# Optimization experiments

Measured on AMD Instinct MI355X. Metric: run time of the kernel, lower is better.

The kernel has to match this reference:

```python
import jax, jax.numpy as jnp
import numpy as np

# Config (matches init_kwargs / input_specs)
H = 128      # hidden_dim
D = 3        # depth (atom message-passing steps)
L = 2        # layers (molecule readout steps)
N = 100000   # total nodes in batch
E = 400000   # total directed edges
G = 5000     # number of graphs (molecules)
FN = 64      # num_atom_type
FE = 16      # num_bond_type


def setup_inputs() -> dict:
    key = jax.random.key(0)
    ks = jax.random.split(key, 32)
    rn = lambda k, shape, s=0.1: jax.random.normal(k, shape, jnp.float32) * s
    inp = {
        'node': rn(ks[0], (N, FN), 1.0),
        'edge': rn(ks[1], (E, FE), 1.0),
        'src': jax.random.randint(ks[2], (E,), 0, N),
        'dst': jax.random.randint(ks[3], (E,), 0, N),
        'graph_ids': jnp.sort(jax.random.randint(ks[4], (N,), 0, G)),
        # input embeddings
        'Wn0': rn(ks[5], (FN, H)), 'bn0': rn(ks[6], (H,)),
        'We0': rn(ks[7], (FE, H)), 'be0': rn(ks[8], (H,)),
        # Atom_AFPLayer params, stacked over depth D
        'aWn': rn(ks[9], (D, H, H)),      'abn': rn(ks[10], (D, H)),
        'aWe': rn(ks[11], (D, 2 * H, H)), 'abe': rn(ks[12], (D, H)),
        'aWal': rn(ks[13], (D, 2 * H, 1)),'abal': rn(ks[14], (D, 1)),
        'aWat': rn(ks[15], (D, H, H)),    'abat': rn(ks[16], (D, H)),
        'aWih': rn(ks[17], (D, H, 3 * H)),'abih': rn(ks[18], (D, 3 * H)),
        'aWhh': rn(ks[19], (D, H, 3 * H)),'abhh': rn(ks[20], (D, 3 * H)),
        # Mol_AFPLayer params, stacked over L
        'mWal': rn(ks[21], (L, 2 * H, 1)),'mbal': rn(ks[22], (L, 1)),
        'mWat': rn(ks[23], (L, H, H)),    'mbat': rn(ks[24], (L, H)),
        'mWih': rn(ks[25], (L, H, 3 * H)),'mbih': rn(ks[26], (L, 3 * H)),
        'mWhh': rn(ks[27], (L, H, 3 * H)),'mbhh': rn(ks[28], (L, 3 * H)),
        # final predictor
        'Wp': rn(ks[29], (H, 1)), 'bp': rn(ks[30], (1,)),
    }
    return inp


def _gru(x, h, Wih, bih, Whh, bhh):
    # torch.nn.GRUCell gate order: r, z, n
    gi = x @ Wih + bih
    gh = h @ Whh + bhh
    ir, iz, inn = jnp.split(gi, 3, axis=-1)
    hr, hz, hn = jnp.split(gh, 3, axis=-1)
    r = jax.nn.sigmoid(ir + hr)
    z = jax.nn.sigmoid(iz + hz)
    n = jnp.tanh(inn + r * hn)
    return (1.0 - z) * n + z * h


def _seg_softmax(score, seg, num):
    # numerically stable softmax within each segment; score: [E,1]
    m = jax.ops.segment_max(score, seg, num_segments=num)
    e = jnp.exp(score - m[seg])
    s = jax.ops.segment_sum(e, seg, num_segments=num)
    return e / s[seg]


def _forward(node, edge, src, dst, graph_ids,
             Wn0, bn0, We0, be0,
             aWn, abn, aWe, abe, aWal, abal, aWat, abat,
             aWih, abih, aWhh, abhh,
             mWal, mbal, mWat, mbat, mWih, mbih, mWhh, mbhh,
             Wp, bp):
    lrelu = jax.nn.leaky_relu  # slope 0.01, same as torch default
    n = lrelu(node @ Wn0 + bn0)   # [N,H] embedded nodes
    e = lrelu(edge @ We0 + be0)   # [E,H] embedded edges (constant across steps)
    Nn = n.shape[0]
    # Atom-level attentive message passing (depth D), per-layer weights
    for d in range(D):
        h = lrelu(n @ aWn[d] + abn[d])                                        # node_embedded_feats
        msg = lrelu(jnp.concatenate([h[src], e], -1) @ aWe[d] + abe[d])       # [E,H] neighbor_message
        score = lrelu(jnp.concatenate([msg, h[dst]], -1) @ aWal[d] + abal[d]) # [E,1]
        att = _seg_softmax(score, dst, Nn)                                    # edge_softmax over dst
        ctx = jax.ops.segment_sum(att * (msg @ aWat[d] + abat[d]), dst, num_segments=Nn)
        ctx = jax.nn.elu(ctx)
        n = jax.nn.relu(_gru(ctx, h, aWih[d], abih[d], aWhh[d], abhh[d]))
    # Molecule-level attentive readout (L steps)
    sn = jax.ops.segment_sum(n, graph_ids, num_segments=G)  # dgl.sum_nodes init
    for l in range(L):
        s = lrelu(sn)
        sc = lrelu(jnp.concatenate([n, s[graph_ids]], -1) @ mWal[l] + mbal[l])  # [N,1]
        aw = _seg_softmax(sc, graph_ids, G)                                     # softmax_nodes
        hid = n @ mWat[l] + mbat[l]
        sctx = jax.nn.elu(jax.ops.segment_sum(aw * hid, graph_ids, num_segments=G))
        sn = jax.nn.relu(_gru(sctx, s, mWih[l], mbih[l], mWhh[l], mbhh[l]))
    return sn @ Wp + bp  # [G,1]


def reference(node, edge, src, dst, graph_ids,
              Wn0, bn0, We0, be0,
              aWn, abn, aWe, abe, aWal, abal, aWat, abat,
              aWih, abih, aWhh, abhh,
              mWal, mbal, mWat, mbat, mWih, mbih, mWhh, mbhh,
              Wp, bp):
    return _forward(node, edge, src, dst, graph_ids,
                    Wn0, bn0, We0, be0,
                    aWn, abn, aWe, abe, aWal, abal, aWat, abat,
                    aWih, abih, aWhh, abhh,
                    mWal, mbal, mWat, mbat, mWih, mbih, mWhh, mbhh,
                    Wp, bp)
```

## Files before the change

kernel.cpp:

```cpp
#include <hip/hip_runtime.h>
#include <hip/hip_bf16.h>
#include <math.h>


#define HD 128
#define H3 384

typedef __attribute__((ext_vector_type(8))) short short8;
typedef __attribute__((ext_vector_type(4))) float f32x4;

__device__ __forceinline__ float lrelu_f(float x) { return x > 0.f ? x : 0.01f * x; }
__device__ __forceinline__ float sigmoid_f(float x) { return 1.f / (1.f + expf(-x)); }

__device__ __forceinline__ void atomicMaxF(float* addr, float val) {
    int iv = __float_as_int(val);
    if (iv >= 0) atomicMax((int*)addr, iv);
    else atomicMin((unsigned int*)addr, (unsigned int)iv);
}

__device__ __forceinline__ unsigned short bf16_rne(float v, float* back) {
    unsigned u = __float_as_uint(v);
    unsigned r = (u + 0x7FFFu + ((u >> 16) & 1u)) >> 16;
    *back = __uint_as_float(r << 16);
    return (unsigned short)r;
}

__device__ __forceinline__ unsigned pack_hl(float v) {
    float back, d;
    unsigned short h = bf16_rne(v, &back);
    unsigned short l = bf16_rne(v - back, &d);
    return ((unsigned)h << 16) | (unsigned)l;
}
__device__ __forceinline__ float unpack_f32(unsigned w) {
    return __uint_as_float(w & 0xffff0000u) + __uint_as_float(w << 16);
}

__device__ __forceinline__ void split8(const float* p, short8& h8, short8& l8) {
    float4 u0 = *reinterpret_cast<const float4*>(p);
    float4 u1 = *reinterpret_cast<const float4*>(p + 4);
    float vv[8] = {u0.x, u0.y, u0.z, u0.w, u1.x, u1.y, u1.z, u1.w};
#pragma unroll
    for (int j = 0; j < 8; ++j) {
        float back, d;
        h8[j] = (short)bf16_rne(vv[j], &back);
        l8[j] = (short)bf16_rne(vv[j] - back, &d);
    }
}

__device__ __forceinline__ void unpack8(const unsigned* p, short8& h8, short8& l8) {
    uint4 w0 = *reinterpret_cast<const uint4*>(p);
    uint4 w1 = *reinterpret_cast<const uint4*>(p + 4);
    unsigned ww[8] = {w0.x, w0.y, w0.z, w0.w, w1.x, w1.y, w1.z, w1.w};
#pragma unroll
    for (int j = 0; j < 8; ++j) {
        h8[j] = (short)(ww[j] >> 16);
        l8[j] = (short)(ww[j] & 0xffffu);
    }
}

__global__ void pack_b_kernel(const float* __restrict__ B, int K, int ldb, int col0,
                              int Ncols, short* __restrict__ hi, short* __restrict__ lo,
                              size_t matB, size_t matO) {
    int KG = 4 * ((K + 31) / 32);
    int mat = blockIdx.y;
    B += (size_t)mat * matB;
    hi += (size_t)mat * matO;
    lo += (size_t)mat * matO;
    int idx = blockIdx.x * blockDim.x + threadIdx.x;
    int total = (Ncols >> 4) * KG * 16;
    if (idx >= total) return;
    int col = idx & 15;
    int kg = (idx >> 4) % KG;
    int nblk = idx / (16 * KG);
    size_t o = (size_t)idx * 8;
#pragma unroll
    for (int e = 0; e < 8; ++e) {
        int k = kg * 8 + e;
        float v = (k < K) ? B[(size_t)k * ldb + col0 + nblk * 16 + col] : 0.f;
        float hf, d;
        unsigned short h = bf16_rne(v, &hf);
        unsigned short l = bf16_rne(v - hf, &d);
        hi[o + e] = (short)h;
        lo[o + e] = (short)l;
    }
}

#define GRU_SL (8 * 16 * 16 * 8)
__global__ void pack_gru_kernel(const float* __restrict__ Wih, const float* __restrict__ Whh,
                                int D, short* __restrict__ hi, short* __restrict__ lo) {
    const int per = 6 * (GRU_SL / 8);
    int idx = blockIdx.x * blockDim.x + threadIdx.x;
    if (idx >= D * per) return;
    int d = idx / per;
    int r = idx % per;
    int s = r / (GRU_SL / 8);
    int g8 = r % (GRU_SL / 8);
    int col = g8 & 15;
    int kg = (g8 >> 4) & 15;
    int nblk = g8 >> 8;
    const float* B = (s < 3 ? Wih : Whh) + (size_t)d * HD * H3;
    int col0 = (s % 3) * HD;
    size_t o = (size_t)idx * 8;
#pragma unroll
    for (int e = 0; e < 8; ++e) {
        int k = kg * 8 + e;
        float v = B[(size_t)k * H3 + col0 + nblk * 16 + col];
        float hf, d2;
        unsigned short h = bf16_rne(v, &hf);
        unsigned short l = bf16_rne(v - hf, &d2);
        hi[o + e] = (short)h;
        lo[o + e] = (short)l;
    }
}

__global__ __launch_bounds__(256) void mfma_gemm(
    const float* __restrict__ A, int K,
    const short* __restrict__ Bhi, const short* __restrict__ Blo, int KG,
    const float* __restrict__ bias, float* __restrict__ C, int M, int N, int act,
    const float* __restrict__ rdw, float* __restrict__ rdout,
    const float* __restrict__ rowmask, int outpk, int apk)
{
    const int t = threadIdx.x, lane = t & 63, w = t >> 6;
    const int wm = w & 1, wn = w >> 1, q = lane >> 4, r16 = lane & 15;
    const int m0 = blockIdx.x * 64, n0 = blockIdx.y * 64;
    const int KT = K >> 5;

    f32x4 acc[2][2];
#pragma unroll
    for (int a = 0; a < 2; ++a)
#pragma unroll
        for (int b = 0; b < 2; ++b) { acc[a][b][0]=0.f; acc[a][b][1]=0.f; acc[a][b][2]=0.f; acc[a][b][3]=0.f; }

    int arow[2];
#pragma unroll
    for (int mt = 0; mt < 2; ++mt) {
        int m = m0 + (wm << 5) + (mt << 4) + r16;
        arow[mt] = (m >= M) ? M - 1 : m;
    }

    for (int kt = 0; kt < KT; ++kt) {
        short8 ah[2], al[2];
#pragma unroll
        for (int mt = 0; mt < 2; ++mt) {
            size_t aoff = (size_t)arow[mt] * K + (kt << 5) + (q << 3);
            if (apk) unpack8((const unsigned*)A + aoff, ah[mt], al[mt]);
            else split8(A + aoff, ah[mt], al[mt]);
        }
        const int kg = (kt << 2) + q;
#pragma unroll
        for (int nt = 0; nt < 2; ++nt) {
            int nblk = (n0 >> 4) + (wn << 1) + nt;
            size_t boff = (((size_t)nblk * KG + kg) * 16 + r16) * 8;
            short8 bh = *reinterpret_cast<const short8*>(Bhi + boff);
            short8 bl = *reinterpret_cast<const short8*>(Blo + boff);
#pragma unroll
            for (int mt = 0; mt < 2; ++mt) {
                acc[mt][nt] = __builtin_amdgcn_mfma_f32_16x16x32_bf16(ah[mt], bh, acc[mt][nt], 0, 0, 0);
                acc[mt][nt] = __builtin_amdgcn_mfma_f32_16x16x32_bf16(ah[mt], bl, acc[mt][nt], 0, 0, 0);
                acc[mt][nt] = __builtin_amdgcn_mfma_f32_16x16x32_bf16(al[mt], bh, acc[mt][nt], 0, 0, 0);
            }
        }
    }

#pragma unroll
    for (int mt = 0; mt < 2; ++mt) {
        float pv[4] = {0.f, 0.f, 0.f, 0.f};
#pragma unroll
        for (int nt = 0; nt < 2; ++nt) {
            int col = n0 + (wn << 5) + (nt << 4) + r16;
            float bi = bias ? bias[col] : 0.f;
            float wc = rdw ? rdw[col] : 0.f;
#pragma unroll
            for (int i = 0; i < 4; ++i) {
                int m = m0 + (wm << 5) + (mt << 4) + (q << 2) + i;
                float v = acc[mt][nt][i] + bi;
                if (act == 1) v = v > 0.f ? v : 0.01f * v;
                else if (act == 2) v = fmaxf(v, 0.f);
                else if (act == 3) v = v > 0.f ? v : expf(v) - 1.f;
                if (rowmask && m < M && rowmask[m] == 0.f) v = 0.f;
                pv[i] += wc * v;
                if (m < M) {
                    if (outpk) ((unsigned*)C)[(size_t)m * N + col] = pack_hl(v);
                    else C[(size_t)m * N + col] = v;
                }
            }
        }
        if (rdw) {
#pragma unroll
            for (int i = 0; i < 4; ++i) {
                float p = pv[i];
                p += __shfl_xor(p, 1); p += __shfl_xor(p, 2);
                p += __shfl_xor(p, 4); p += __shfl_xor(p, 8);
                int m = m0 + (wm << 5) + (mt << 4) + (q << 2) + i;
                if (r16 == 0 && m < M) atomicAdd(&rdout[m], p);
            }
        }
    }
}

__global__ __launch_bounds__(256) void msg_pass_kernel(
    const unsigned* __restrict__ hpk, const int* __restrict__ srcp,
    const int* __restrict__ dstp, const int* __restrict__ eidp,
    const float* __restrict__ edge,
    const short* __restrict__ W0hi, const short* __restrict__ W0lo,
    const float* __restrict__ be0,
    const short* __restrict__ Wehi, const short* __restrict__ Welo,
    const float* __restrict__ be,
    const float* __restrict__ wal,
    float* __restrict__ sc, float* __restrict__ S,
    void* __restrict__ msgpk, int fullprec,
    int E, int mode)
{
    __shared__ unsigned int elds[64 * 128];
    const int t = threadIdx.x, lane = t & 63, w = t >> 6;
    const int wm = w & 1, wn = w >> 1, q = lane >> 4, r16 = lane & 15;
    const int e0 = blockIdx.x * 64;

    {
        f32x4 ea[2][4];
#pragma unroll
        for (int a = 0; a < 2; ++a)
#pragma unroll
            for (int b = 0; b < 4; ++b) { ea[a][b][0]=0.f; ea[a][b][1]=0.f; ea[a][b][2]=0.f; ea[a][b][3]=0.f; }
        short8 eah[2], eal[2];
#pragma unroll
        for (int mt = 0; mt < 2; ++mt) {
            int er = e0 + (wm << 5) + (mt << 4) + r16;
            if (er >= E) er = E - 1;
            int eid = eidp[er];
            if (q < 2) split8(edge + (size_t)eid * 16 + (q << 3), eah[mt], eal[mt]);
            else {
#pragma unroll
                for (int j = 0; j < 8; ++j) { eah[mt][j] = 0; eal[mt][j] = 0; }
            }
        }
#pragma unroll
        for (int nt = 0; nt < 4; ++nt) {
            int nblk = (wn << 2) + nt;
            size_t boff = (((size_t)nblk * 4 + q) * 16 + r16) * 8;
            short8 bh = *reinterpret_cast<const short8*>(W0hi + boff);
            short8 bl = *reinterpret_cast<const short8*>(W0lo + boff);
#pragma unroll
            for (int mt = 0; mt < 2; ++mt) {
                ea[mt][nt] = __builtin_amdgcn_mfma_f32_16x16x32_bf16(eah[mt], bh, ea[mt][nt], 0, 0, 0);
                ea[mt][nt] = __builtin_amdgcn_mfma_f32_16x16x32_bf16(eah[mt], bl, ea[mt][nt], 0, 0, 0);
                ea[mt][nt] = __builtin_amdgcn_mfma_f32_16x16x32_bf16(eal[mt], bh, ea[mt][nt], 0, 0, 0);
            }
        }
#pragma unroll
        for (int mt = 0; mt < 2; ++mt)
#pragma unroll
            for (int nt = 0; nt < 4; ++nt) {
                int col = (wn << 6) + (nt << 4) + r16;
#pragma unroll
                for (int i = 0; i < 4; ++i) {
                    int row = (wm << 5) + (mt << 4) + (q << 2) + i;
                    float v = lrelu_f(ea[mt][nt][i] + be0[col]);
                    elds[row * 128 + (col ^ ((row & 7) << 2))] = pack_hl(v);
                }
            }
    }
    __syncthreads();

    f32x4 acc[2][4];
#pragma unroll
    for (int a = 0; a < 2; ++a)
#pragma unroll
        for (int b = 0; b < 4; ++b) { acc[a][b][0]=0.f; acc[a][b][1]=0.f; acc[a][b][2]=0.f; acc[a][b][3]=0.f; }
    int grow[2], arw[2];
#pragma unroll
    for (int mt = 0; mt < 2; ++mt) {
        int m = e0 + (wm << 5) + (mt << 4) + r16;
        if (m >= E) m = E - 1;
        grow[mt] = srcp[m];
        arw[mt] = (wm << 5) + (mt << 4) + r16;
    }
#pragma unroll
    for (int kt = 0; kt < 8; ++kt) {
        short8 ah[2], al[2];
#pragma unroll
        for (int mt = 0; mt < 2; ++mt) {
            if (kt < 4) {
                unpack8(hpk + (size_t)grow[mt] * HD + (kt << 5) + (q << 3), ah[mt], al[mt]);
            } else {
                int row = arw[mt];
                int sh = (row & 7) << 2;
                int c = ((kt - 4) << 5) + (q << 3);
                uint4 w0 = *reinterpret_cast<const uint4*>(&elds[row * 128 + (c ^ sh)]);
                uint4 w1 = *reinterpret_cast<const uint4*>(&elds[row * 128 + ((c + 4) ^ sh)]);
                unsigned ww[8] = {w0.x, w0.y, w0.z, w0.w, w1.x, w1.y, w1.z, w1.w};
#pragma unroll
                for (int j = 0; j < 8; ++j) {
                    ah[mt][j] = (short)(ww[j] >> 16);
                    al[mt][j] = (short)(ww[j] & 0xffffu);
                }
            }
        }
        const int kg = (kt << 2) + q;
#pragma unroll
        for (int nt = 0; nt < 4; ++nt) {
            int nblk = (wn << 2) + nt;
            size_t boff = (((size_t)nblk * 32 + kg) * 16 + r16) * 8;
            short8 bh = *reinterpret_cast<const short8*>(Wehi + boff);
            short8 bl = *reinterpret_cast<const short8*>(Welo + boff);
#pragma unroll
            for (int mt = 0; mt < 2; ++mt) {
                acc[mt][nt] = __builtin_amdgcn_mfma_f32_16x16x32_bf16(ah[mt], bh, acc[mt][nt], 0, 0, 0);
                acc[mt][nt] = __builtin_amdgcn_mfma_f32_16x16x32_bf16(ah[mt], bl, acc[mt][nt], 0, 0, 0);
                acc[mt][nt] = __builtin_amdgcn_mfma_f32_16x16x32_bf16(al[mt], bh, acc[mt][nt], 0, 0, 0);
            }
        }
    }

    if (mode == 2) {
#pragma unroll
        for (int mt = 0; mt < 2; ++mt)
#pragma unroll
            for (int i = 0; i < 4; ++i) {
                int m = e0 + (wm << 5) + (mt << 4) + (q << 2) + i;
                if (m >= E) continue;
                float a = sc[m];
                int dn = dstp[m];
#pragma unroll
                for (int nt = 0; nt < 4; ++nt) {
                    int col = (wn << 6) + (nt << 4) + r16;
                    float v = lrelu_f(acc[mt][nt][i] + be[col]);
                    atomicAdd(&S[(size_t)dn * HD + col], a * v);
                }
            }
        return;
    }

#pragma unroll
    for (int mt = 0; mt < 2; ++mt) {
        float pv[4] = {0.f, 0.f, 0.f, 0.f};
#pragma unroll
        for (int i = 0; i < 4; ++i) {
            int m = e0 + (wm << 5) + (mt << 4) + (q << 2) + i;
#pragma unroll
            for (int nt = 0; nt < 4; ++nt) {
                int col = (wn << 6) + (nt << 4) + r16;
                float v = lrelu_f(acc[mt][nt][i] + be[col]);
                pv[i] += wal[col] * v;
                if (mode == 0 && m < E) {
                    size_t ro = (size_t)m * HD + col;
                    if (fullprec) ((unsigned*)msgpk)[ro] = pack_hl(v);
                    else { float b_; ((unsigned short*)msgpk)[ro] = bf16_rne(v, &b_); }
                }
            }
        }
#pragma unroll
        for (int i = 0; i < 4; ++i) {
            float p = pv[i];
            p += __shfl_xor(p, 1); p += __shfl_xor(p, 2);
            p += __shfl_xor(p, 4); p += __shfl_xor(p, 8);
            int m = e0 + (wm << 5) + (mt << 4) + (q << 2) + i;
            if (r16 == 0 && m < E) atomicAdd(&sc[m], p);
        }
    }
}

__global__ __launch_bounds__(256) void ctx_gather_kernel(
    const void* __restrict__ msgpk, const float* __restrict__ sc,
    const int* __restrict__ rowptr, unsigned* __restrict__ Spk, int Nn, int fullprec)
{
    int wid = (blockIdx.x * blockDim.x + threadIdx.x) >> 6;
    int lane = threadIdx.x & 63;
    if (wid >= Nn) return;
    int p0 = rowptr[wid], p1 = rowptr[wid + 1];
    float a0 = 0.f, a1 = 0.f;
    if (fullprec) {
        const unsigned* mp = (const unsigned*)msgpk;
        for (int p = p0; p < p1; ++p) {
            float a = sc[p];
            uint2 w = *reinterpret_cast<const uint2*>(mp + (size_t)p * HD + lane * 2);
            a0 += a * unpack_f32(w.x);
            a1 += a * unpack_f32(w.y);
        }
    } else {
        const unsigned short* mp = (const unsigned short*)msgpk;
        for (int p = p0; p < p1; ++p) {
            float a = sc[p];
            unsigned w = *reinterpret_cast<const unsigned*>(mp + (size_t)p * HD + lane * 2);
            a0 += a * __uint_as_float(w << 16);
            a1 += a * __uint_as_float(w & 0xffff0000u);
        }
    }
    Spk[(size_t)wid * HD + lane * 2] = pack_hl(a0);
    Spk[(size_t)wid * HD + lane * 2 + 1] = pack_hl(a1);
}

__global__ void hist_kernel(const int* __restrict__ dst, int* __restrict__ cnt, int E) {
    int i = blockIdx.x * blockDim.x + threadIdx.x;
    if (i < E) atomicAdd(&cnt[dst[i]], 1);
}
__global__ void scan1_kernel(const int* __restrict__ cnt, int* __restrict__ pre,
                             int* __restrict__ btot, int total) {
    __shared__ int ts[256];
    int base = blockIdx.x * 1024;
    int c[4], tsum = 0;
#pragma unroll
    for (int j = 0; j < 4; ++j) {
        int idx = base + threadIdx.x * 4 + j;
        c[j] = (idx < total) ? cnt[idx] : 0;
        tsum += c[j];
    }
    ts[threadIdx.x] = tsum;
    __syncthreads();
    for (int off = 1; off < 256; off <<= 1) {
        int v = (threadIdx.x >= off) ? ts[threadIdx.x - off] : 0;
        __syncthreads();
        ts[threadIdx.x] += v;
        __syncthreads();
    }
    int run = ts[threadIdx.x] - tsum;
#pragma unroll
    for (int j = 0; j < 4; ++j) {
        int idx = base + threadIdx.x * 4 + j;
        if (idx < total) pre[idx] = run;
        run += c[j];
    }
    if (threadIdx.x == 255) btot[blockIdx.x] = ts[255];
}
__global__ void scan2_kernel(int* __restrict__ btot, int nb) {
    __shared__ int ts[256];
    int v = (threadIdx.x < nb) ? btot[threadIdx.x] : 0;
    ts[threadIdx.x] = v;
    __syncthreads();
    for (int off = 1; off < 256; off <<= 1) {
        int u = (threadIdx.x >= off) ? ts[threadIdx.x - off] : 0;
        __syncthreads();
        ts[threadIdx.x] += u;
        __syncthreads();
    }
    if (threadIdx.x < nb) btot[threadIdx.x] = ts[threadIdx.x] - v;
}
__global__ void scan3_kernel(int* __restrict__ pre, const int* __restrict__ btot, int total) {
    int i = blockIdx.x * blockDim.x + threadIdx.x;
    if (i < total) pre[i] += btot[i >> 10];
}
__global__ void fill_kernel(const int* __restrict__ src, const int* __restrict__ dst,
                            const int* __restrict__ rowptr, int* __restrict__ fillc,
                            int* __restrict__ srcp, int* __restrict__ dstp,
                            int* __restrict__ eidp, int E) {
    int i = blockIdx.x * blockDim.x + threadIdx.x;
    if (i >= E) return;
    int d = dst[i];
    int pos = rowptr[d] + atomicAdd(&fillc[d], 1);
    srcp[pos] = src[i];
    dstp[pos] = d;
    eidp[pos] = i;
}

__global__ __launch_bounds__(256) void gru_fused_kernel(
    const unsigned* __restrict__ ctxpk, const unsigned* __restrict__ hpk,
    const short* __restrict__ ghi, const short* __restrict__ glo,
    const float* __restrict__ bih, const float* __restrict__ bhh,
    unsigned* __restrict__ out, int M)
{
    const int t = threadIdx.x, lane = t & 63, w = t >> 6;
    const int wm = w & 1, wn = w >> 1, q = lane >> 4, r16 = lane & 15;
    const int m0 = blockIdx.x * 64, j0 = blockIdx.y * 64;

    f32x4 acc[6][2][2];
#pragma unroll
    for (int g = 0; g < 6; ++g)
#pragma unroll
        for (int a = 0; a < 2; ++a)
#pragma unroll
            for (int b = 0; b < 2; ++b) { acc[g][a][b][0]=0.f; acc[g][a][b][1]=0.f; acc[g][a][b][2]=0.f; acc[g][a][b][3]=0.f; }

    int arow[2];
#pragma unroll
    for (int mt = 0; mt < 2; ++mt) {
        int m = m0 + (wm << 5) + (mt << 4) + r16;
        arow[mt] = (m >= M) ? M - 1 : m;
    }

#pragma unroll
    for (int kt = 0; kt < 4; ++kt) {
        short8 ah[2], al[2];
#pragma unroll
        for (int mt = 0; mt < 2; ++mt)
            unpack8(ctxpk + (size_t)arow[mt] * HD + (kt << 5) + (q << 3), ah[mt], al[mt]);
        const int kg = (kt << 2) + q;
#pragma unroll
        for (int g = 0; g < 3; ++g)
#pragma unroll
            for (int nt = 0; nt < 2; ++nt) {
                int nblk = (j0 >> 4) + (wn << 1) + nt;
                size_t boff = (size_t)g * GRU_SL + (((size_t)nblk * 16 + kg) * 16 + r16) * 8;
                short8 bh = *reinterpret_cast<const short8*>(ghi + boff);
                short8 bl = *reinterpret_cast<const short8*>(glo + boff);
#pragma unroll
                for (int mt = 0; mt < 2; ++mt) {
                    acc[g][mt][nt] = __builtin_amdgcn_mfma_f32_16x16x32_bf16(ah[mt], bh, acc[g][mt][nt], 0, 0, 0);
                    acc[g][mt][nt] = __builtin_amdgcn_mfma_f32_16x16x32_bf16(ah[mt], bl, acc[g][mt][nt], 0, 0, 0);
                    acc[g][mt][nt] = __builtin_amdgcn_mfma_f32_16x16x32_bf16(al[mt], bh, acc[g][mt][nt], 0, 0, 0);
                }
            }
    }
#pragma unroll
    for (int kt = 0; kt < 4; ++kt) {
        short8 ah[2], al[2];
#pragma unroll
        for (int mt = 0; mt < 2; ++mt)
            unpack8(hpk + (size_t)arow[mt] * HD + (kt << 5) + (q << 3), ah[mt], al[mt]);
        const int kg = (kt << 2) + q;
#pragma unroll
        for (int g = 3; g < 6; ++g)
#pragma unroll
            for (int nt = 0; nt < 2; ++nt) {
                int nblk = (j0 >> 4) + (wn << 1) + nt;
                size_t boff = (size_t)g * GRU_SL + (((size_t)nblk * 16 + kg) * 16 + r16) * 8;
                short8 bh = *reinterpret_cast<const short8*>(ghi + boff);
                short8 bl = *reinterpret_cast<const short8*>(glo + boff);
#pragma unroll
                for (int mt = 0; mt < 2; ++mt) {
                    acc[g][mt][nt] = __builtin_amdgcn_mfma_f32_16x16x32_bf16(ah[mt], bh, acc[g][mt][nt], 0, 0, 0);
                    acc[g][mt][nt] = __builtin_amdgcn_mfma_f32_16x16x32_bf16(ah[mt], bl, acc[g][mt][nt], 0, 0, 0);
                    acc[g][mt][nt] = __builtin_amdgcn_mfma_f32_16x16x32_bf16(al[mt], bh, acc[g][mt][nt], 0, 0, 0);
                }
            }
    }

#pragma unroll
    for (int mt = 0; mt < 2; ++mt)
#pragma unroll
        for (int nt = 0; nt < 2; ++nt) {
            int j = j0 + (wn << 5) + (nt << 4) + r16;
            float bir = bih[j], biz = bih[HD + j], bin = bih[2 * HD + j];
            float bhr = bhh[j], bhz = bhh[HD + j], bhn = bhh[2 * HD + j];
#pragma unroll
            for (int i = 0; i < 4; ++i) {
                int m = m0 + (wm << 5) + (mt << 4) + (q << 2) + i;
                if (m >= M) continue;
                float r = sigmoid_f(acc[0][mt][nt][i] + bir + acc[3][mt][nt][i] + bhr);
                float z = sigmoid_f(acc[1][mt][nt][i] + biz + acc[4][mt][nt][i] + bhz);
                float hn = acc[5][mt][nt][i] + bhn;
                float nn = tanhf(acc[2][mt][nt][i] + bin + r * hn);
                float hv = unpack_f32(hpk[(size_t)m * HD + j]);
                out[(size_t)m * HD + j] = pack_hl(fmaxf((1.f - z) * nn + z * hv, 0.f));
            }
        }
}

__global__ void init_maxsum_kernel(float* mx, float* sm, int n) {
    int i = blockIdx.x * blockDim.x + threadIdx.x;
    if (i < n) { mx[i] = -__builtin_inff(); sm[i] = 0.f; }
}

__global__ void score_combine_kernel(float* __restrict__ sc, const float* __restrict__ hd2,
                                     const int* __restrict__ seg, const float* __restrict__ bal,
                                     float* __restrict__ maxbuf, int count) {
    int i = blockIdx.x * blockDim.x + threadIdx.x;
    if (i >= count) return;
    int s = seg[i];
    float v = lrelu_f(sc[i] + hd2[s] + bal[0]);
    sc[i] = v;
    atomicMaxF(&maxbuf[s], v);
}

__global__ __launch_bounds__(256) void score_kernel(
    const unsigned* __restrict__ Apk, const float* __restrict__ B,
    const int* __restrict__ seg, const float* __restrict__ w,
    const float* __restrict__ bal, float* __restrict__ out,
    float* __restrict__ maxbuf, int count)
{
    int i = (blockIdx.x * blockDim.x + threadIdx.x) >> 6;
    int lane = threadIdx.x & 63;
    if (i >= count) return;
    int s = seg[i];
    float a0 = unpack_f32(Apk[(size_t)i * HD + lane]);
    float a1 = unpack_f32(Apk[(size_t)i * HD + lane + 64]);
    const float* br = B + (size_t)s * HD;
    float p = a0 * w[lane] + a1 * w[lane + 64]
            + br[lane] * w[128 + lane] + br[lane + 64] * w[192 + lane];
#pragma unroll
    for (int off = 32; off > 0; off >>= 1) p += __shfl_down(p, off);
    if (lane == 0) {
        float v = lrelu_f(p + bal[0]);
        out[i] = v;
        atomicMaxF(&maxbuf[s], v);
    }
}

__global__ void expsum_kernel(float* __restrict__ sc, const float* __restrict__ mx,
                              float* __restrict__ sm, const int* __restrict__ seg, int count) {
    int i = blockIdx.x * blockDim.x + threadIdx.x;
    if (i >= count) return;
    int s = seg[i];
    float p = expf(sc[i] - mx[s]);
    sc[i] = p;
    atomicAdd(&sm[s], p);
}

__global__ void attdiv_kernel(float* __restrict__ sc, const float* __restrict__ sm,
                              const int* __restrict__ seg, int count) {
    int i = blockIdx.x * blockDim.x + threadIdx.x;
    if (i >= count) return;
    sc[i] = sc[i] / sm[seg[i]];
}

__global__ void gru_gate_kernel(const float* __restrict__ gi, const float* __restrict__ gh,
                                const float* __restrict__ h, float* __restrict__ out, int M) {
    size_t idx = (size_t)blockIdx.x * blockDim.x + threadIdx.x;
    if (idx >= (size_t)M * HD) return;
    size_t row = idx >> 7; int col = (int)(idx & 127);
    const float* gir = gi + row * H3;
    const float* ghr = gh + row * H3;
    float r = sigmoid_f(gir[col] + ghr[col]);
    float z = sigmoid_f(gir[col + 128] + ghr[col + 128]);
    float nn = tanhf(gir[col + 256] + r * ghr[col + 256]);
    float o = (1.f - z) * nn + z * h[idx];
    out[idx] = fmaxf(o, 0.f);
}

__global__ void lrelu_copy_kernel(const float* __restrict__ in, float* __restrict__ out, size_t n) {
    size_t i = (size_t)blockIdx.x * blockDim.x + threadIdx.x;
    if (i >= n) return;
    out[i] = lrelu_f(in[i]);
}

__global__ void segsum_kernel(const unsigned* __restrict__ npk, const int* __restrict__ gid,
                              float* __restrict__ sn, int Nn) {
    size_t idx = (size_t)blockIdx.x * blockDim.x + threadIdx.x;
    if (idx >= (size_t)Nn * HD) return;
    size_t row = idx >> 7; int col = (int)(idx & 127);
    atomicAdd(&sn[(size_t)gid[row] * HD + col], unpack_f32(npk[idx]));
}

__global__ void seg_scale_sum_kernel(const unsigned* __restrict__ npk, const int* __restrict__ gid,
                                     const float* __restrict__ scale, float* __restrict__ out, int Nn) {
    size_t idx = (size_t)blockIdx.x * blockDim.x + threadIdx.x;
    if (idx >= (size_t)Nn * HD) return;
    size_t row = idx >> 7; int col = (int)(idx & 127);
    atomicAdd(&out[(size_t)gid[row] * HD + col], scale[row] * unpack_f32(npk[idx]));
}

__global__ void final_kernel(const float* __restrict__ sn, const float* __restrict__ Wp,
                             const float* __restrict__ bp, float* __restrict__ out, int G) {
    int g = (blockIdx.x * blockDim.x + threadIdx.x) >> 6;
    int lane = threadIdx.x & 63;
    if (g >= G) return;
    const float* r = sn + (size_t)g * HD;
    float p = r[lane] * Wp[lane] + r[lane + 64] * Wp[lane + 64];
#pragma unroll
    for (int off = 32; off > 0; off >>= 1) p += __shfl_down(p, off);
    if (lane == 0) out[g] = p + bp[0];
}

__global__ void canary_kernel(float* out, int n) {
    int i = blockIdx.x * blockDim.x + threadIdx.x;
    if (i < n) out[i] = 123.456f;
}

struct PkB { const short* hi; const short* lo; int KG; };

extern "C" void kernel_launch(void* const* d_in, const int* in_sizes, int n_in,
                              void* d_out, int out_size, void* d_ws, size_t ws_size,
                              hipStream_t stream) {
    const float* node = (const float*)d_in[0];
    const float* edge = (const float*)d_in[1];
    const int*   src  = (const int*)d_in[2];
    const int*   dst  = (const int*)d_in[3];
    const int*   gid  = (const int*)d_in[4];
    const float* Wn0  = (const float*)d_in[5];
    const float* bn0  = (const float*)d_in[6];
    const float* We0  = (const float*)d_in[7];
    const float* be0  = (const float*)d_in[8];
    const float* aWn  = (const float*)d_in[9];
    const float* abn  = (const float*)d_in[10];
    const float* aWe  = (const float*)d_in[11];
    const float* abe  = (const float*)d_in[12];
    const float* aWal = (const float*)d_in[13];
    const float* abal = (const float*)d_in[14];
    const float* aWat = (const float*)d_in[15];
    const float* abat = (const float*)d_in[16];
    const float* aWih = (const float*)d_in[17];
    const float* abih = (const float*)d_in[18];
    const float* aWhh = (const float*)d_in[19];
    const float* abhh = (const float*)d_in[20];
    const float* mWal = (const float*)d_in[21];
    const float* mbal = (const float*)d_in[22];
    const float* mWat = (const float*)d_in[23];
    const float* mbat = (const float*)d_in[24];
    const float* mWih = (const float*)d_in[25];
    const float* mbih = (const float*)d_in[26];
    const float* mWhh = (const float*)d_in[27];
    const float* mbhh = (const float*)d_in[28];
    const float* Wp   = (const float*)d_in[29];
    const float* bp   = (const float*)d_in[30];

    const int N = in_sizes[0] / 64;
    const int E = in_sizes[1] / 16;
    const int G = out_size;
    const int D = in_sizes[9] / (HD * HD);
    const int L = in_sizes[21] / (2 * HD);
    if (D > 8 || L > 4) return;

    char* wsb = (char*)d_ws;

    short* pkcur = (short*)wsb;
    size_t elN;
    auto packBn = [&](const float* B, int K, int ldb, int col0, int Ncols,
                      int nmat, size_t matB) -> PkB {
        int KG = 4 * ((K + 31) / 32);
        size_t elems = (size_t)(Ncols >> 4) * KG * 16 * 8;
        elN = elems;
        short* hi = pkcur; pkcur += elems * nmat;
        short* lo = pkcur; pkcur += elems * nmat;
        int total = (Ncols >> 4) * KG * 16;
        dim3 g((total + 255) / 256, nmat);
        pack_b_kernel<<<g, 256, 0, stream>>>(B, K, ldb, col0, Ncols, hi, lo, matB, elems);
        PkB p; p.hi = hi; p.lo = lo; p.KG = KG; return p;
    };
    PkB pWe0 = packBn(We0, 16, HD, 0, HD, 1, 0);
    PkB pWn0 = packBn(Wn0, 64, HD, 0, HD, 1, 0);
    PkB pAWn[8], pAWe[8], pAWat[8];
    {
        PkB b = packBn(aWn, HD, HD, 0, HD, D, (size_t)HD * HD);
        for (int d = 0; d < D; ++d) { pAWn[d] = b; pAWn[d].hi = b.hi + d * elN; pAWn[d].lo = b.lo + d * elN; }
        b = packBn(aWe, 2 * HD, HD, 0, HD, D, (size_t)2 * HD * HD);
        for (int d = 0; d < D; ++d) { pAWe[d] = b; pAWe[d].hi = b.hi + d * elN; pAWe[d].lo = b.lo + d * elN; }
        b = packBn(aWat, HD, HD, 0, HD, D, (size_t)HD * HD);
        for (int d = 0; d < D; ++d) { pAWat[d] = b; pAWat[d].hi = b.hi + d * elN; pAWat[d].lo = b.lo + d * elN; }
    }
    short* ghiAll = pkcur; pkcur += (size_t)D * 6 * GRU_SL;
    short* gloAll = pkcur; pkcur += (size_t)D * 6 * GRU_SL;
    {
        int total = D * 6 * (GRU_SL / 8);
        pack_gru_kernel<<<(total + 255) / 256, 256, 0, stream>>>(aWih, aWhh, D, ghiAll, gloAll);
    }
    const short *gHi[8], *gLo[8];
    for (int d = 0; d < D; ++d) {
        gHi[d] = ghiAll + (size_t)d * 6 * GRU_SL;
        gLo[d] = gloAll + (size_t)d * 6 * GRU_SL;
    }
    PkB pMWat[4], pMWih[4], pMWhh[4];
    {
        PkB b = packBn(mWat, HD, HD, 0, HD, L, (size_t)HD * HD);
        for (int l = 0; l < L; ++l) { pMWat[l] = b; pMWat[l].hi = b.hi + l * elN; pMWat[l].lo = b.lo + l * elN; }
        b = packBn(mWih, HD, H3, 0, H3, L, (size_t)HD * H3);
        for (int l = 0; l < L; ++l) { pMWih[l] = b; pMWih[l].hi = b.hi + l * elN; pMWih[l].lo = b.lo + l * elN; }
        b = packBn(mWhh, HD, H3, 0, H3, L, (size_t)HD * H3);
        for (int l = 0; l < L; ++l) { pMWhh[l] = b; pMWhh[l].hi = b.hi + l * elN; pMWhh[l].lo = b.lo + l * elN; }
    }

    size_t off = ((size_t)((char*)pkcur - wsb) + 255) & ~(size_t)255;
    auto alloc = [&](size_t bytes) -> void* {
        void* p = (void*)(wsb + off);
        off += (bytes + 255) & ~(size_t)255;
        return p;
    };
    unsigned* npk = (unsigned*)alloc((size_t)N * HD * 4);
    unsigned* hpk = (unsigned*)alloc((size_t)N * HD * 4);
    float* sc_e = (float*)alloc((size_t)E * 4);
    float* nmax = (float*)alloc((size_t)N * 4);
    float* nsum = (float*)alloc((size_t)N * 4);
    float* sc_n = (float*)alloc((size_t)N * 4);
    float* hd2  = (float*)alloc((size_t)N * 4);
    float* sn   = (float*)alloc((size_t)G * HD * 4);
    float* gmax = (float*)alloc((size_t)G * 4);
    float* gsum = (float*)alloc((size_t)G * 4);
    int* cnt    = (int*)alloc((size_t)(N + 1) * 4);
    int* rowptr = (int*)alloc((size_t)(N + 1) * 4);
    int* fillc  = (int*)alloc((size_t)N * 4);
    int* srcp   = (int*)alloc((size_t)E * 4);
    int* dstp   = (int*)alloc((size_t)E * 4);
    int* eidp   = (int*)alloc((size_t)E * 4);
    int* btot   = (int*)alloc(1024 * 4);

    size_t ovr_off = off;
    size_t ctx_bytes = (size_t)N * HD * 4;
    size_t mol_bytes = 3 * ((size_t)G * HD * 4 + 256) + 2 * ((size_t)G * H3 * 4 + 256);
    size_t min_ovr = ctx_bytes > mol_bytes ? ctx_bytes : mol_bytes;
    int csr_mode, fullprec = 0;
    size_t mf = (size_t)E * HD * 4, mh = (size_t)E * HD * 2;
    if (ovr_off + (mf > min_ovr ? mf : min_ovr) <= ws_size) { csr_mode = 1; fullprec = 1; }
    else if (ovr_off + (mh > min_ovr ? mh : min_ovr) <= ws_size) { csr_mode = 1; fullprec = 0; }
    else if (ovr_off + min_ovr <= ws_size) { csr_mode = 0; }
    else {
        canary_kernel<<<(G + 255) / 256, 256, 0, stream>>>((float*)d_out, G);
        return;
    }
    void*     msgpk = (void*)(wsb + ovr_off);
    unsigned* ctxpk = (unsigned*)(wsb + ovr_off);
    size_t mo = ovr_off;
    auto molalloc = [&](size_t bytes) -> float* {
        float* p = (float*)(wsb + mo);
        mo += (bytes + 255) & ~(size_t)255;
        return p;
    };
    float* sbuf = molalloc((size_t)G * HD * 4);
    float* sctx = molalloc((size_t)G * HD * 4);
    float* Sg   = molalloc((size_t)G * HD * 4);
    float* gim  = molalloc((size_t)G * H3 * 4);
    float* ghm  = molalloc((size_t)G * H3 * 4);

    const int total_sc = N + 1;
    const int nb = (total_sc + 1023) / 1024;
    if (nb > 256) {
        canary_kernel<<<(G + 255) / 256, 256, 0, stream>>>((float*)d_out, G);
        return;
    }

    auto mgemm = [&](const void* A, int K, const PkB& pk, const float* bias, void* C,
                     int M, int Nc, int act, const float* rdw, float* rdout,
                     const float* rowmask, int outpk, int apk) {
        dim3 g((M + 63) / 64, Nc / 64);
        mfma_gemm<<<g, dim3(256), 0, stream>>>((const float*)A, K, pk.hi, pk.lo, pk.KG,
                                               bias, (float*)C, M, Nc, act, rdw, rdout,
                                               rowmask, outpk, apk);
    };

    hipMemsetAsync(cnt, 0, (size_t)(N + 1) * 4, stream);
    hipMemsetAsync(fillc, 0, (size_t)N * 4, stream);
    hist_kernel<<<(E + 255) / 256, 256, 0, stream>>>(dst, cnt, E);
    scan1_kernel<<<nb, 256, 0, stream>>>(cnt, rowptr, btot, total_sc);
    scan2_kernel<<<1, 256, 0, stream>>>(btot, nb);
    scan3_kernel<<<(total_sc + 255) / 256, 256, 0, stream>>>(rowptr, btot, total_sc);
    fill_kernel<<<(E + 255) / 256, 256, 0, stream>>>(src, dst, rowptr, fillc,
                                                     srcp, dstp, eidp, E);

    mgemm(node, 64, pWn0, bn0, npk, N, HD, 1, nullptr, nullptr, nullptr, 1, 0);

    const int EB = (E + 63) / 64;
    for (int d = 0; d < D; ++d) {
        const float* bn_d  = abn  + (size_t)d * HD;
        const float* be_d  = abe  + (size_t)d * HD;
        const float* Wal_d = aWal + (size_t)d * 2 * HD;
        const float* bal_d = abal + d;
        const float* bat_d = abat + (size_t)d * HD;
        const float* bih_d = abih + (size_t)d * H3;
        const float* bhh_d = abhh + (size_t)d * H3;

        hipMemsetAsync(hd2, 0, (size_t)N * 4, stream);
        hipMemsetAsync(sc_e, 0, (size_t)E * 4, stream);
        mgemm(npk, HD, pAWn[d], bn_d, hpk, N, HD, 1, Wal_d + HD, hd2, nullptr, 1, 1);
        init_maxsum_kernel<<<(N + 255) / 256, 256, 0, stream>>>(nmax, nsum, N);
        msg_pass_kernel<<<EB, 256, 0, stream>>>(hpk, srcp, dstp, eidp, edge,
                                                pWe0.hi, pWe0.lo, be0,
                                                pAWe[d].hi, pAWe[d].lo, be_d, Wal_d,
                                                sc_e, nullptr, msgpk, fullprec, E,
                                                csr_mode ? 0 : 1);
        score_combine_kernel<<<(E + 255) / 256, 256, 0, stream>>>(sc_e, hd2, dstp, bal_d, nmax, E);
        expsum_kernel<<<(E + 255) / 256, 256, 0, stream>>>(sc_e, nmax, nsum, dstp, E);
        attdiv_kernel<<<(E + 255) / 256, 256, 0, stream>>>(sc_e, nsum, dstp, E);
        if (csr_mode) {
            ctx_gather_kernel<<<(N + 3) / 4, 256, 0, stream>>>(msgpk, sc_e, rowptr,
                                                               npk, N, fullprec);
        } else {
            hipMemsetAsync(npk, 0, (size_t)N * HD * 4, stream);
            msg_pass_kernel<<<EB, 256, 0, stream>>>(hpk, srcp, dstp, eidp, edge,
                                                    pWe0.hi, pWe0.lo, be0,
                                                    pAWe[d].hi, pAWe[d].lo, be_d, nullptr,
                                                    sc_e, (float*)npk, nullptr, 0, E, 2);
        }
        mgemm(npk, HD, pAWat[d], bat_d, ctxpk, N, HD, 3, nullptr, nullptr, nsum, 1,
              csr_mode ? 1 : 0);
        dim3 gg((N + 63) / 64, 2);
        gru_fused_kernel<<<gg, dim3(256), 0, stream>>>(ctxpk, hpk, gHi[d], gLo[d],
                                                       bih_d, bhh_d, npk, N);
    }

    hipMemsetAsync(sn, 0, (size_t)G * HD * 4, stream);
    segsum_kernel<<<((size_t)N * HD + 255) / 256, 256, 0, stream>>>(npk, gid, sn, N);
    for (int l = 0; l < L; ++l) {
        const float* Wal_l = mWal + (size_t)l * 2 * HD;
        const float* bal_l = mbal + l;
        const float* bat_l = mbat + (size_t)l * HD;
        const float* bih_l = mbih + (size_t)l * H3;
        const float* bhh_l = mbhh + (size_t)l * H3;

        lrelu_copy_kernel<<<((size_t)G * HD + 255) / 256, 256, 0, stream>>>(sn, sbuf, (size_t)G * HD);
        init_maxsum_kernel<<<(G + 255) / 256, 256, 0, stream>>>(gmax, gsum, G);
        score_kernel<<<(N + 3) / 4, 256, 0, stream>>>(npk, sbuf, gid, Wal_l, bal_l, sc_n, gmax, N);
        expsum_kernel<<<(N + 255) / 256, 256, 0, stream>>>(sc_n, gmax, gsum, gid, N);
        attdiv_kernel<<<(N + 255) / 256, 256, 0, stream>>>(sc_n, gsum, gid, N);
        hipMemsetAsync(Sg, 0, (size_t)G * HD * 4, stream);
        seg_scale_sum_kernel<<<((size_t)N * HD + 255) / 256, 256, 0, stream>>>(npk, gid, sc_n, Sg, N);
        mgemm(Sg, HD, pMWat[l], bat_l, sctx, G, HD, 3, nullptr, nullptr, gsum, 0, 0);
        mgemm(sctx, HD, pMWih[l], bih_l, gim, G, H3, 0, nullptr, nullptr, nullptr, 0, 0);
        mgemm(sbuf, HD, pMWhh[l], bhh_l, ghm, G, H3, 0, nullptr, nullptr, nullptr, 0, 0);
        gru_gate_kernel<<<((size_t)G * HD + 255) / 256, 256, 0, stream>>>(gim, ghm, sbuf, sn, G);
    }

    final_kernel<<<(G + 3) / 4, 256, 0, stream>>>(sn, Wp, bp, (float*)d_out, G);
}
```

Measured before the change: 1.845 ms.

## Fuse attention softmax into message-pass epilogue and drop edge-embedding low half

The edge-score combine, exp and segment-sum steps move into the msg_pass epilogue. The softmax max-subtraction is dropped, and normalization by the segment sum is deferred to the consumers (ctx gather, mode-2 scatter, seg_scale_sum). This removes several E- and N-sized elementwise kernels, the max-init kernels and a memset per step. The two column-halves of the score are now reduced through shared memory instead of global atomics. Edge embeddings are also stored in LDS as single bf16 instead of hi/lo pairs, which removes one MFMA per tile for that half, at the cost of lower precision and a softmax that could overflow without max subtraction.

```diff
diff --git a/kernel.cpp b/kernel.cpp
--- a/kernel.cpp
+++ b/kernel.cpp
@@ -11,12 +11,6 @@
 
 __device__ __forceinline__ float lrelu_f(float x) { return x > 0.f ? x : 0.01f * x; }
 __device__ __forceinline__ float sigmoid_f(float x) { return 1.f / (1.f + expf(-x)); }
-
-__device__ __forceinline__ void atomicMaxF(float* addr, float val) {
-    int iv = __float_as_int(val);
-    if (iv >= 0) atomicMax((int*)addr, iv);
-    else atomicMin((unsigned int*)addr, (unsigned int)iv);
-}
 
 __device__ __forceinline__ unsigned short bf16_rne(float v, float* back) {
     unsigned u = __float_as_uint(v);
@@ -206,12 +200,14 @@
     const float* __restrict__ be0,
     const short* __restrict__ Wehi, const short* __restrict__ Welo,
     const float* __restrict__ be,
-    const float* __restrict__ wal,
-    float* __restrict__ sc, float* __restrict__ S,
+    const float* __restrict__ wal, const float* __restrict__ hd2,
+    const float* __restrict__ bal,
+    float* __restrict__ sc, float* __restrict__ nsum, float* __restrict__ S,
     void* __restrict__ msgpk, int fullprec,
     int E, int mode)
 {
-    __shared__ unsigned int elds[64 * 128];
+    __shared__ unsigned short elds[64 * 128];
+    __shared__ float sred[64];
     const int t = threadIdx.x, lane = t & 63, w = t >> 6;
     const int wm = w & 1, wn = w >> 1, q = lane >> 4, r16 = lane & 15;
     const int e0 = blockIdx.x * 64;
@@ -256,7 +252,8 @@
                 for (int i = 0; i < 4; ++i) {
                     int row = (wm << 5) + (mt << 4) + (q << 2) + i;
                     float v = lrelu_f(ea[mt][nt][i] + be0[col]);
-                    elds[row * 128 + (col ^ ((row & 7) << 2))] = pack_hl(v);
+                    float b_;
+                    elds[row * 128 + (col ^ ((row & 7) << 3))] = bf16_rne(v, &b_);
                 }
             }
     }
@@ -278,21 +275,22 @@
 #pragma unroll
     for (int kt = 0; kt < 8; ++kt) {
         short8 ah[2], al[2];
+        const bool ehalf = (kt >= 4);
 #pragma unroll
         for (int mt = 0; mt < 2; ++mt) {
-            if (kt < 4) {
+            if (!ehalf) {
                 unpack8(hpk + (size_t)grow[mt] * HD + (kt << 5) + (q << 3), ah[mt], al[mt]);
             } else {
                 int row = arw[mt];
-                int sh = (row & 7) << 2;
+                int sh = (row & 7) << 3;
                 int c = ((kt - 4) << 5) + (q << 3);
-                uint4 w0 = *reinterpret_cast<const uint4*>(&elds[row * 128 + (c ^ sh)]);
-                uint4 w1 = *reinterpret_cast<const uint4*>(&elds[row * 128 + ((c + 4) ^ sh)]);
-                unsigned ww[8] = {w0.x, w0.y, w0.z, w0.w, w1.x, w1.y, w1.z, w1.w};
-#pragma unroll
-                for (int j = 0; j < 8; ++j) {
-                    ah[mt][j] = (short)(ww[j] >> 16);
-                    al[mt][j] = (short)(ww[j] & 0xffffu);
+                uint4 wv = *reinterpret_cast<const uint4*>(&elds[row * 128 + (c ^ sh)]);
+                unsigned ww[4] = {wv.x, wv.y, wv.z, wv.w};
+#pragma unroll
+                for (int j = 0; j < 4; ++j) {
+                    ah[mt][2 * j]     = (short)(ww[j] & 0xffffu);
+                    ah[mt][2 * j + 1] = (short)(ww[j] >> 16);
+                    al[mt][2 * j] = 0; al[mt][2 * j + 1] = 0;
                 }
             }
         }
@@ -307,7 +305,8 @@
             for (int mt = 0; mt < 2; ++mt) {
                 acc[mt][nt] = __builtin_amdgcn_mfma_f32_16x16x32_bf16(ah[mt], bh, acc[mt][nt], 0, 0, 0);
                 acc[mt][nt] = __builtin_amdgcn_mfma_f32_16x16x32_bf16(ah[mt], bl, acc[mt][nt], 0, 0, 0);
-                acc[mt][nt] = __builtin_amdgcn_mfma_f32_16x16x32_bf16(al[mt], bh, acc[mt][nt], 0, 0, 0);
+                if (!ehalf)
+                    acc[mt][nt] = __builtin_amdgcn_mfma_f32_16x16x32_bf16(al[mt], bh, acc[mt][nt], 0, 0, 0);
             }
         }
     }
@@ -319,8 +318,9 @@
             for (int i = 0; i < 4; ++i) {
                 int m = e0 + (wm << 5) + (mt << 4) + (q << 2) + i;
                 if (m >= E) continue;
-                float a = sc[m];
                 int dn = dstp[m];
+                float s = nsum[dn];
+                float a = (s > 0.f) ? sc[m] / s : 0.f;
 #pragma unroll
                 for (int nt = 0; nt < 4; ++nt) {
                     int col = (wn << 6) + (nt << 4) + r16;
@@ -331,9 +331,11 @@
         return;
     }
 
+    float pv[2][4];
 #pragma unroll
     for (int mt = 0; mt < 2; ++mt) {
-        float pv[4] = {0.f, 0.f, 0.f, 0.f};
+#pragma unroll
+        for (int i = 0; i < 4; ++i) pv[mt][i] = 0.f;
 #pragma unroll
         for (int i = 0; i < 4; ++i) {
             int m = e0 + (wm << 5) + (mt << 4) + (q << 2) + i;
@@ -341,7 +343,7 @@
             for (int nt = 0; nt < 4; ++nt) {
                 int col = (wn << 6) + (nt << 4) + r16;
                 float v = lrelu_f(acc[mt][nt][i] + be[col]);
-                pv[i] += wal[col] * v;
+                pv[mt][i] += wal[col] * v;
                 if (mode == 0 && m < E) {
                     size_t ro = (size_t)m * HD + col;
                     if (fullprec) ((unsigned*)msgpk)[ro] = pack_hl(v);
@@ -351,28 +353,54 @@
         }
 #pragma unroll
         for (int i = 0; i < 4; ++i) {
-            float p = pv[i];
+            float p = pv[mt][i];
             p += __shfl_xor(p, 1); p += __shfl_xor(p, 2);
             p += __shfl_xor(p, 4); p += __shfl_xor(p, 8);
-            int m = e0 + (wm << 5) + (mt << 4) + (q << 2) + i;
-            if (r16 == 0 && m < E) atomicAdd(&sc[m], p);
-        }
+            pv[mt][i] = p;
+        }
+    }
+    if (wn == 0 && r16 == 0) {
+#pragma unroll
+        for (int mt = 0; mt < 2; ++mt)
+#pragma unroll
+            for (int i = 0; i < 4; ++i)
+                sred[(wm << 5) + (mt << 4) + (q << 2) + i] = pv[mt][i];
+    }
+    __syncthreads();
+    if (wn == 1 && r16 == 0) {
+#pragma unroll
+        for (int mt = 0; mt < 2; ++mt)
+#pragma unroll
+            for (int i = 0; i < 4; ++i) {
+                int row = (wm << 5) + (mt << 4) + (q << 2) + i;
+                int m = e0 + row;
+                if (m < E) {
+                    int dm = dstp[m];
+                    float v = lrelu_f(pv[mt][i] + sred[row] + hd2[dm] + bal[0]);
+                    float e = expf(v);
+                    sc[m] = e;
+                    atomicAdd(&nsum[dm], e);
+                }
+            }
     }
 }
 
 __global__ __launch_bounds__(256) void ctx_gather_kernel(
     const void* __restrict__ msgpk, const float* __restrict__ sc,
-    const int* __restrict__ rowptr, unsigned* __restrict__ Spk, int Nn, int fullprec)
+    const float* __restrict__ nsum, const int* __restrict__ rowptr,
+    unsigned* __restrict__ Spk, int Nn, int fullprec)
 {
     int wid = (blockIdx.x * blockDim.x + threadIdx.x) >> 6;
     int lane = threadIdx.x & 63;
     if (wid >= Nn) return;
     int p0 = rowptr[wid], p1 = rowptr[wid + 1];
+    float s = nsum[wid];
+    float inv = (s > 0.f) ? 1.f / s : 0.f;
     float a0 = 0.f, a1 = 0.f;
     if (fullprec) {
         const unsigned* mp = (const unsigned*)msgpk;
         for (int p = p0; p < p1; ++p) {
-            float a = sc[p];
+            float a = sc[p] * inv;
             uint2 w = *reinterpret_cast<const uint2*>(mp + (size_t)p * HD + lane * 2);
             a0 += a * unpack_f32(w.x);
             a1 += a * unpack_f32(w.y);
@@ -380,7 +408,7 @@
     } else {
         const unsigned short* mp = (const unsigned short*)msgpk;
         for (int p = p0; p < p1; ++p) {
-            float a = sc[p];
+            float a = sc[p] * inv;
             unsigned w = *reinterpret_cast<const unsigned*>(mp + (size_t)p * HD + lane * 2);
             a0 += a * __uint_as_float(w << 16);
             a1 += a * __uint_as_float(w & 0xffff0000u);
@@ -545,27 +573,11 @@
         }
 }
 
-__global__ void init_maxsum_kernel(float* mx, float* sm, int n) {
-    int i = blockIdx.x * blockDim.x + threadIdx.x;
-    if (i < n) { mx[i] = -__builtin_inff(); sm[i] = 0.f; }
-}
-
-__global__ void score_combine_kernel(float* __restrict__ sc, const float* __restrict__ hd2,
-                                     const int* __restrict__ seg, const float* __restrict__ bal,
-                                     float* __restrict__ maxbuf, int count) {
-    int i = blockIdx.x * blockDim.x + threadIdx.x;
-    if (i >= count) return;
-    int s = seg[i];
-    float v = lrelu_f(sc[i] + hd2[s] + bal[0]);
-    sc[i] = v;
-    atomicMaxF(&maxbuf[s], v);
-}
-
 __global__ __launch_bounds__(256) void score_kernel(
     const unsigned* __restrict__ Apk, const float* __restrict__ B,
     const int* __restrict__ seg, const float* __restrict__ w,
     const float* __restrict__ bal, float* __restrict__ out,
-    float* __restrict__ maxbuf, int count)
+    float* __restrict__ sumbuf, int count)
 {
     int i = (blockIdx.x * blockDim.x + threadIdx.x) >> 6;
     int lane = threadIdx.x & 63;
@@ -579,27 +591,10 @@
 #pragma unroll
     for (int off = 32; off > 0; off >>= 1) p += __shfl_down(p, off);
     if (lane == 0) {
-        float v = lrelu_f(p + bal[0]);
-        out[i] = v;
-        atomicMaxF(&maxbuf[s], v);
-    }
-}
-
-__global__ void expsum_kernel(float* __restrict__ sc, const float* __restrict__ mx,
-                              float* __restrict__ sm, const int* __restrict__ seg, int count) {
-    int i = blockIdx.x * blockDim.x + threadIdx.x;
-    if (i >= count) return;
-    int s = seg[i];
-    float p = expf(sc[i] - mx[s]);
-    sc[i] = p;
-    atomicAdd(&sm[s], p);
-}
-
-__global__ void attdiv_kernel(float* __restrict__ sc, const float* __restrict__ sm,
-                              const int* __restrict__ seg, int count) {
-    int i = blockIdx.x * blockDim.x + threadIdx.x;
-    if (i >= count) return;
-    sc[i] = sc[i] / sm[seg[i]];
+        float e = expf(lrelu_f(p + bal[0]));
+        out[i] = e;
+        atomicAdd(&sumbuf[s], e);
+    }
 }
 
 __global__ void gru_gate_kernel(const float* __restrict__ gi, const float* __restrict__ gh,
@@ -631,11 +626,15 @@
 }
 
 __global__ void seg_scale_sum_kernel(const unsigned* __restrict__ npk, const int* __restrict__ gid,
-                                     const float* __restrict__ scale, float* __restrict__ out, int Nn) {
+                                     const float* __restrict__ scale, const float* __restrict__ gsum,
+                                     float* __restrict__ out, int Nn) {
     size_t idx = (size_t)blockIdx.x * blockDim.x + threadIdx.x;
     if (idx >= (size_t)Nn * HD) return;
     size_t row = idx >> 7; int col = (int)(idx & 127);
-    atomicAdd(&out[(size_t)gid[row] * HD + col], scale[row] * unpack_f32(npk[idx]));
+    int g = gid[row];
+    float s = gsum[g];
+    float a = (s > 0.f) ? scale[row] / s : 0.f;
+    atomicAdd(&out[(size_t)g * HD + col], a * unpack_f32(npk[idx]));
 }
 
 __global__ void final_kernel(const float* __restrict__ sn, const float* __restrict__ Wp,
@@ -756,12 +755,11 @@
     unsigned* npk = (unsigned*)alloc((size_t)N * HD * 4);
     unsigned* hpk = (unsigned*)alloc((size_t)N * HD * 4);
     float* sc_e = (float*)alloc((size_t)E * 4);
-    float* nmax = (float*)alloc((size_t)N * 4);
-    float* nsum = (float*)alloc((size_t)N * 4);
+    float* zn   = (float*)alloc((size_t)2 * N * 4);
+    float* hd2  = zn;
+    float* nsum = zn + N;
     float* sc_n = (float*)alloc((size_t)N * 4);
-    float* hd2  = (float*)alloc((size_t)N * 4);
     float* sn   = (float*)alloc((size_t)G * HD * 4);
-    float* gmax = (float*)alloc((size_t)G * 4);
     float* gsum = (float*)alloc((size_t)G * 4);
     int* cnt    = (int*)alloc((size_t)(N + 1) * 4);
     int* rowptr = (int*)alloc((size_t)(N + 1) * 4);
@@ -835,27 +833,24 @@
         const float* bih_d = abih + (size_t)d * H3;
         const float* bhh_d = abhh + (size_t)d * H3;
 
-        hipMemsetAsync(hd2, 0, (size_t)N * 4, stream);
-        hipMemsetAsync(sc_e, 0, (size_t)E * 4, stream);
+        hipMemsetAsync(zn, 0, (size_t)2 * N * 4, stream);
         mgemm(npk, HD, pAWn[d], bn_d, hpk, N, HD, 1, Wal_d + HD, hd2, nullptr, 1, 1);
-        init_maxsum_kernel<<<(N + 255) / 256, 256, 0, stream>>>(nmax, nsum, N);
         msg_pass_kernel<<<EB, 256, 0, stream>>>(hpk, srcp, dstp, eidp, edge,
                                                 pWe0.hi, pWe0.lo, be0,
-                                                pAWe[d].hi, pAWe[d].lo, be_d, Wal_d,
-                                                sc_e, nullptr, msgpk, fullprec, E,
+                                                pAWe[d].hi, pAWe[d].lo, be_d,
+                                                Wal_d, hd2, bal_d,
+                                                sc_e, nsum, nullptr, msgpk, fullprec, E,
                                                 csr_mode ? 0 : 1);
-        score_combine_kernel<<<(E + 255) / 256, 256, 0, stream>>>(sc_e, hd2, dstp, bal_d, nmax, E);
-        expsum_kernel<<<(E + 255) / 256, 256, 0, stream>>>(sc_e, nmax, nsum, dstp, E);
-        attdiv_kernel<<<(E + 255) / 256, 256, 0, stream>>>(sc_e, nsum, dstp, E);
         if (csr_mode) {
-            ctx_gather_kernel<<<(N + 3) / 4, 256, 0, stream>>>(msgpk, sc_e, rowptr,
+            ctx_gather_kernel<<<(N + 3) / 4, 256, 0, stream>>>(msgpk, sc_e, nsum, rowptr,
                                                                npk, N, fullprec);
         } else {
             hipMemsetAsync(npk, 0, (size_t)N * HD * 4, stream);
             msg_pass_kernel<<<EB, 256, 0, stream>>>(hpk, srcp, dstp, eidp, edge,
                                                     pWe0.hi, pWe0.lo, be0,
-                                                    pAWe[d].hi, pAWe[d].lo, be_d, nullptr,
-                                                    sc_e, (float*)npk, nullptr, 0, E, 2);
+                                                    pAWe[d].hi, pAWe[d].lo, be_d,
+                                                    Wal_d, hd2, bal_d,
+                                                    sc_e, nsum, (float*)npk, nullptr, 0, E, 2);
         }
         mgemm(npk, HD, pAWat[d], bat_d, ctxpk, N, HD, 3, nullptr, nullptr, nsum, 1,
               csr_mode ? 1 : 0);
@@ -874,12 +869,10 @@
         const float* bhh_l = mbhh + (size_t)l * H3;
 
         lrelu_copy_kernel<<<((size_t)G * HD + 255) / 256, 256, 0, stream>>>(sn, sbuf, (size_t)G * HD);
-        init_maxsum_kernel<<<(G + 255) / 256, 256, 0, stream>>>(gmax, gsum, G);
-        score_kernel<<<(N + 3) / 4, 256, 0, stream>>>(npk, sbuf, gid, Wal_l, bal_l, sc_n, gmax, N);
-        expsum_kernel<<<(N + 255) / 256, 256, 0, stream>>>(sc_n, gmax, gsum, gid, N);
-        attdiv_kernel<<<(N + 255) / 256, 256, 0, stream>>>(sc_n, gsum, gid, N);
+        hipMemsetAsync(gsum, 0, (size_t)G * 4, stream);
+        score_kernel<<<(N + 3) / 4, 256, 0, stream>>>(npk, sbuf, gid, Wal_l, bal_l, sc_n, gsum, N);
         hipMemsetAsync(Sg, 0, (size_t)G * HD * 4, stream);
-        seg_scale_sum_kernel<<<((size_t)N * HD + 255) / 256, 256, 0, stream>>>(npk, gid, sc_n, Sg, N);
+        seg_scale_sum_kernel<<<((size_t)N * HD + 255) / 256, 256, 0, stream>>>(npk, gid, sc_n, gsum, Sg, N);
         mgemm(Sg, HD, pMWat[l], bat_l, sctx, G, HD, 3, nullptr, nullptr, gsum, 0, 0);
         mgemm(sctx, HD, pMWih[l], bih_l, gim, G, H3, 0, nullptr, nullptr, nullptr, 0, 0);
         mgemm(sbuf, HD, pMWhh[l], bhh_l, ghm, G, H3, 0, nullptr, nullptr, nullptr, 0, 0);
```

Result: faster. 1.787 ms (median of 2 runs) (-3.2%).
